# Optimization experiments

Hardware: AMD Instinct MI355X
Metric: run time of the kernel (lower is better)

## Reference

```python
import jax, jax.numpy as jnp
import numpy as np

IN_F = 1024   # in_features
OUT_F = 1024  # out_features
N = 32768     # flattened batch (prod of x.shape[:-1]))
K = 3         # clones per rewire -> denom = K + 1


def setup_inputs() -> dict:
    key = jax.random.key(0)
    k1, k2, k3, k4 = jax.random.split(key, 4)
    bound = 1.0 / np.sqrt(IN_F)
    x = jax.random.normal(k1, (N, IN_F), dtype=jnp.float32)
    # kaiming-uniform-ish init scale for weight, uniform(-bound,bound) for bias
    weight = jax.random.uniform(k2, (OUT_F, IN_F), dtype=jnp.float32,
                                minval=-bound, maxval=bound) * np.sqrt(3.0)
    bias = jax.random.uniform(k3, (OUT_F,), dtype=jnp.float32,
                              minval=-bound, maxval=bound)
    # one rewire per output row; clones are distinct from src (dead-neuron slots)
    rewire_rows = jnp.arange(OUT_F, dtype=jnp.int32)
    rewire_src = jax.random.randint(k4, (OUT_F,), 0, IN_F, dtype=jnp.int32)
    rewire_clones = (rewire_src[:, None] + jnp.arange(1, K + 1, dtype=jnp.int32)) % IN_F
    return {"x": x, "weight": weight, "bias": bias,
            "rewire_rows": rewire_rows, "rewire_src": rewire_src,
            "rewire_clones": rewire_clones}


def reference(x, weight, bias, rewire_rows, rewire_src, rewire_clones):
    # Plain linear part, shared by all output rows: y = x @ W^T + b
    base = x @ weight.T + bias                                  # [N, OUT_F]

    # Per-rewire correction. For rewire e on row r with src s and clones d_k
    # (denom = K+1), the torch loop replaces x[:, s] -> x[:, s]/denom and
    # x[:, d_k] -> x[:, s]/denom before the GEMV with weight[r].
    # Equivalent delta added to base[:, r] (indices within a rewire are disjoint):
    denom = rewire_clones.shape[1] + 1                          # K + 1
    xs = x[:, rewire_src]                                       # [N, R]
    new_val = xs / denom                                        # [N, R]
    w_src = weight[rewire_rows, rewire_src]                     # [R]
    delta = (new_val - xs) * w_src                              # src column change
    xc = x[:, rewire_clones]                                    # [N, R, K]
    wc = weight[rewire_rows[:, None], rewire_clones]            # [R, K]
    delta = delta + jnp.einsum('nrk,rk->nr', new_val[:, :, None] - xc, wc)

    # Scatter-add the deltas into their output rows (duplicates accumulate).
    return base.at[:, rewire_rows].add(delta)                   # [N, OUT_F]
```

## Files before the change

### kernel.cpp

```cpp
#include <hip/hip_runtime.h>

#define IN_F 1024
#define OUT_F 1024
#define NTOK 32768
#define BM 256
#define BN 256
#define BK 64
#define KT (IN_F / BK)

typedef __bf16 bf16;
typedef __bf16 bf16x4 __attribute__((ext_vector_type(4)));
typedef __bf16 bf16x8 __attribute__((ext_vector_type(8)));
typedef float f32x4 __attribute__((ext_vector_type(4)));

__global__ void build_wp(const float* __restrict__ W,
                         const int* __restrict__ rows,
                         const int* __restrict__ srcs,
                         const int* __restrict__ clones,
                         bf16* __restrict__ Wp) {
  const int r = blockIdx.x;
  const int row = rows[r];
  const int s = srcs[r];
  const int c0 = clones[3 * r + 0];
  const int c1 = clones[3 * r + 1];
  const int c2 = clones[3 * r + 2];
  const float* wr = W + (size_t)row * IN_F;
  const float fixv = 0.25f * (wr[s] + wr[c0] + wr[c1] + wr[c2]);

  const int col = threadIdx.x * 4;
  f32x4 v = *reinterpret_cast<const f32x4*>(wr + col);
  bf16x4 o;
#pragma unroll
  for (int j = 0; j < 4; ++j) {
    const int c = col + j;
    float f = v[j];
    if (c == c0 || c == c1 || c == c2) f = 0.0f;
    if (c == s) f = fixv;
    o[j] = (bf16)f;
  }
  *reinterpret_cast<bf16x4*>(Wp + (size_t)row * IN_F + col) = o;
}

__global__ __launch_bounds__(512, 2) void gemm_rewire(
    const float* __restrict__ X, const bf16* __restrict__ Wp,
    const float* __restrict__ bias, float* __restrict__ out) {
  extern __shared__ __align__(16) char smem[];

  const int tid = threadIdx.x;
  const int lane = tid & 63;
  const int w = tid >> 6;
  const int wrow = w >> 2;
  const int wcol = w & 3;

  const int bid = blockIdx.x;
  const int sq = bid >> 3;
  const int bm = (bid & 7) + 8 * (sq >> 2);
  const int bn = sq & 3;

  const float* gA = X + ((size_t)bm * BM + (tid >> 3)) * IN_F + (tid & 7) * 8;
  const int awbyte =
      ((tid >> 3) << 7) + ((((tid & 7) ^ ((tid >> 3) & 7))) << 4);

  const bf16* gB = Wp + ((size_t)bn * BN + w * 8 + (lane >> 3)) * IN_F +
                   (((lane & 7) ^ ((lane >> 3) & 7)) << 3);

  f32x4 acc[8][4];
#pragma unroll
  for (int n = 0; n < 4; ++n) {
    const float bv = bias[bn * BN + wcol * 64 + n * 16 + (lane & 15)];
#pragma unroll
    for (int m = 0; m < 8; ++m) acc[m][n] = (f32x4){bv, bv, bv, bv};
  }

  const int arow0 = wrow * 128 + (lane & 15);
  const int brow0 = wcol * 64 + (lane & 15);
  const int sl0 = lane >> 4;
  const int lx7 = lane & 7;

  f32x4 av[8];

  auto issueA = [&](int t) {
#pragma unroll
    for (int j = 0; j < 4; ++j) {
      const float* p = gA + (size_t)j * 64 * IN_F + (size_t)t * BK;
      av[2 * j] = *reinterpret_cast<const f32x4*>(p);
      av[2 * j + 1] = *reinterpret_cast<const f32x4*>(p + 4);
    }
  };
  auto writeA = [&](int buf) {
    char* base = smem + buf * 32768;
#pragma unroll
    for (int j = 0; j < 4; ++j) {
      bf16x8 o;
#pragma unroll
      for (int q = 0; q < 4; ++q) {
        o[q] = (bf16)av[2 * j][q];
        o[4 + q] = (bf16)av[2 * j + 1][q];
      }
      *reinterpret_cast<bf16x8*>(base + j * 8192 + awbyte) = o;
    }
  };
  auto issueB = [&](int t, int buf) {
    const bf16* g = gB + (size_t)t * BK;
    char* dst0 = smem + 65536 + buf * 32768 + w * 1024;
#pragma unroll
    for (int i = 0; i < 4; ++i) {
      __builtin_amdgcn_global_load_lds(
          (const __attribute__((address_space(1))) void*)(g +
                                                          (size_t)i * 64 * IN_F),
          (__attribute__((address_space(3))) void*)(dst0 + i * 8192), 16, 0, 0);
    }
  };
  auto compute = [&](int buf) {
    const char* A = smem + buf * 32768;
    const char* B = smem + 65536 + buf * 32768;
#pragma unroll
    for (int kk = 0; kk < 2; ++kk) {
      const int sl = sl0 + kk * 4;
      const int so = ((sl ^ lx7) << 4);
      bf16x8 af[8], bfr[4];
#pragma unroll
      for (int m = 0; m < 8; ++m)
        af[m] =
            *reinterpret_cast<const bf16x8*>(A + (arow0 + m * 16) * 128 + so);
#pragma unroll
      for (int n = 0; n < 4; ++n)
        bfr[n] =
            *reinterpret_cast<const bf16x8*>(B + (brow0 + n * 16) * 128 + so);
      __builtin_amdgcn_s_setprio(1);
#pragma unroll
      for (int m = 0; m < 8; ++m)
#pragma unroll
        for (int n = 0; n < 4; ++n)
          acc[m][n] = __builtin_amdgcn_mfma_f32_16x16x32_bf16(
              af[m], bfr[n], acc[m][n], 0, 0, 0);
      __builtin_amdgcn_s_setprio(0);
    }
  };

  issueA(0);
  issueB(0, 0);
  writeA(0);
  __syncthreads();

  for (int t = 0; t < KT; ++t) {
    const int db = t & 1;
    const bool more = (t + 1) < KT;
    if (more) {
      issueA(t + 1);
      issueB(t + 1, db ^ 1);
      __builtin_amdgcn_sched_barrier(0);
    }
    compute(db);
    if (more) {
      __builtin_amdgcn_sched_barrier(0);
      writeA(db ^ 1);
      __syncthreads();
    }
  }

  const int orow0 = bm * BM + wrow * 128 + (lane >> 4) * 4;
  const int ocol = bn * BN + wcol * 64 + (lane & 15);
#pragma unroll
  for (int m = 0; m < 8; ++m) {
#pragma unroll
    for (int n = 0; n < 4; ++n) {
      const f32x4 v = acc[m][n];
      const size_t base = (size_t)(orow0 + m * 16) * OUT_F + (ocol + n * 16);
#pragma unroll
      for (int i = 0; i < 4; ++i) out[base + (size_t)i * OUT_F] = v[i];
    }
  }
}

extern "C" void kernel_launch(void* const* d_in, const int* in_sizes, int n_in,
                              void* d_out, int out_size, void* d_ws,
                              size_t ws_size, hipStream_t stream) {
  const float* x = (const float*)d_in[0];
  const float* weight = (const float*)d_in[1];
  const float* bias = (const float*)d_in[2];
  const int* rrows = (const int*)d_in[3];
  const int* rsrc = (const int*)d_in[4];
  const int* rclones = (const int*)d_in[5];
  float* out = (float*)d_out;
  bf16* Wp = (bf16*)d_ws;

  (void)hipFuncSetAttribute((const void*)gemm_rewire,
                            hipFuncAttributeMaxDynamicSharedMemorySize, 131072);

  build_wp<<<dim3(OUT_F), dim3(256), 0, stream>>>(weight, rrows, rsrc, rclones,
                                                  Wp);
  gemm_rewire<<<dim3((NTOK / BM) * (OUT_F / BN)), dim3(512), 131072, stream>>>(
      x, Wp, bias, out);
}
```

Baseline: 106.3 us.

## Restructure GEMM main loop into fine-grained phased pipeline with manual waitcnts

Replaces the simple double-buffered K loop with a hand-scheduled loop unrolled by two K tiles. Each tile is split into four MFMA phases, and the A global loads, A LDS writes and B async LDS loads are interleaved in halves between those phases. Synchronisation uses explicit s_barrier and s_waitcnt vmcnt/lgkmcnt instead of __syncthreads. A is prefetched two tiles ahead in registers. The aim is to hide global latency and LDS traffic behind MFMA work, at the cost of more registers and fragile manual wait counts.

After: 105.6 us. Within noise of the previous version (-0.6%).

```diff
diff --git a/kernel.cpp b/kernel.cpp
--- a/kernel.cpp
+++ b/kernel.cpp
@@ -7,11 +7,17 @@
 #define BN 256
 #define BK 64
 #define KT (IN_F / BK)
+#define NITER (KT / 2)
 
 typedef __bf16 bf16;
 typedef __bf16 bf16x4 __attribute__((ext_vector_type(4)));
 typedef __bf16 bf16x8 __attribute__((ext_vector_type(8)));
 typedef float f32x4 __attribute__((ext_vector_type(4)));
+
+#define LDS_A0 0
+#define LDS_A1 32768
+#define LDS_B0 65536
+#define LDS_B1 98304
 
 __global__ void build_wp(const float* __restrict__ W,
                          const int* __restrict__ rows,
@@ -62,7 +68,7 @@
       ((tid >> 3) << 7) + ((((tid & 7) ^ ((tid >> 3) & 7))) << 4);
 
   const bf16* gB = Wp + ((size_t)bn * BN + w * 8 + (lane >> 3)) * IN_F +
-                   (((lane & 7) ^ ((lane >> 3) & 7)) << 3);
+                   (((lane & 7) ^ ((lane >> 3) & 7)) * 8);
 
   f32x4 acc[8][4];
 #pragma unroll
@@ -72,92 +78,140 @@
     for (int m = 0; m < 8; ++m) acc[m][n] = (f32x4){bv, bv, bv, bv};
   }
 
-  const int arow0 = wrow * 128 + (lane & 15);
-  const int brow0 = wcol * 64 + (lane & 15);
+  const int rl = lane & 15;
+  const int rx = rl & 7;
+  const int arow0 = wrow * 128 + rl;
+  const int brow0 = wcol * 64 + rl;
   const int sl0 = lane >> 4;
-  const int lx7 = lane & 7;
-
-  f32x4 av[8];
-
-  auto issueA = [&](int t) {
-#pragma unroll
-    for (int j = 0; j < 4; ++j) {
-      const float* p = gA + (size_t)j * 64 * IN_F + (size_t)t * BK;
-      av[2 * j] = *reinterpret_cast<const f32x4*>(p);
-      av[2 * j + 1] = *reinterpret_cast<const f32x4*>(p + 4);
-    }
-  };
-  auto writeA = [&](int buf) {
-    char* base = smem + buf * 32768;
-#pragma unroll
-    for (int j = 0; j < 4; ++j) {
+
+  bf16x8 bfr[4][2];
+  f32x4 aH0[4], aH1[4], aP0[4], aP1[4];
+
+  auto loadAhalf = [&](int t, int h, f32x4 (&v)[4]) {
+#pragma unroll
+    for (int jj = 0; jj < 2; ++jj) {
+      const float* p = gA + (size_t)(2 * h + jj) * 64 * IN_F + (size_t)t * BK;
+      v[2 * jj] = *reinterpret_cast<const f32x4*>(p);
+      v[2 * jj + 1] = *reinterpret_cast<const f32x4*>(p + 4);
+    }
+  };
+  auto writeAhalf = [&](int bufOff, int h, const f32x4 (&v)[4]) {
+#pragma unroll
+    for (int jj = 0; jj < 2; ++jj) {
       bf16x8 o;
 #pragma unroll
       for (int q = 0; q < 4; ++q) {
-        o[q] = (bf16)av[2 * j][q];
-        o[4 + q] = (bf16)av[2 * j + 1][q];
+        o[q] = (bf16)v[2 * jj][q];
+        o[4 + q] = (bf16)v[2 * jj + 1][q];
       }
-      *reinterpret_cast<bf16x8*>(base + j * 8192 + awbyte) = o;
-    }
-  };
-  auto issueB = [&](int t, int buf) {
-    const bf16* g = gB + (size_t)t * BK;
-    char* dst0 = smem + 65536 + buf * 32768 + w * 1024;
-#pragma unroll
-    for (int i = 0; i < 4; ++i) {
+      *reinterpret_cast<bf16x8*>(smem + bufOff + (2 * h + jj) * 8192 + awbyte) =
+          o;
+    }
+  };
+  auto issueBhalf = [&](int t, int bufOff, int h) {
+#pragma unroll
+    for (int ii = 0; ii < 2; ++ii) {
+      const int i = 2 * h + ii;
       __builtin_amdgcn_global_load_lds(
-          (const __attribute__((address_space(1))) void*)(g +
+          (const __attribute__((address_space(1))) void*)(gB + (size_t)t * BK +
                                                           (size_t)i * 64 * IN_F),
-          (__attribute__((address_space(3))) void*)(dst0 + i * 8192), 16, 0, 0);
-    }
-  };
-  auto compute = [&](int buf) {
-    const char* A = smem + buf * 32768;
-    const char* B = smem + 65536 + buf * 32768;
-#pragma unroll
-    for (int kk = 0; kk < 2; ++kk) {
-      const int sl = sl0 + kk * 4;
-      const int so = ((sl ^ lx7) << 4);
-      bf16x8 af[8], bfr[4];
-#pragma unroll
-      for (int m = 0; m < 8; ++m)
-        af[m] =
-            *reinterpret_cast<const bf16x8*>(A + (arow0 + m * 16) * 128 + so);
+          (__attribute__((address_space(3))) void*)(smem + bufOff + i * 8192 +
+                                                    w * 1024),
+          16, 0, 0);
+    }
+  };
+  auto readB = [&](int bufOff) {
+#pragma unroll
+    for (int n = 0; n < 4; ++n)
+#pragma unroll
+      for (int kk = 0; kk < 2; ++kk)
+        bfr[n][kk] = *reinterpret_cast<const bf16x8*>(
+            smem + bufOff + (brow0 + n * 16) * 128 +
+            (((kk * 4 + sl0) ^ rx) << 4));
+  };
+  auto phase = [&](int bufAOff, int m2, int ew) {
+    bf16x8 af[2][2];
+#pragma unroll
+    for (int dm = 0; dm < 2; ++dm)
+#pragma unroll
+      for (int kk = 0; kk < 2; ++kk)
+        af[dm][kk] = *reinterpret_cast<const bf16x8*>(
+            smem + bufAOff + (arow0 + (m2 + dm) * 16) * 128 +
+            (((kk * 4 + sl0) ^ rx) << 4));
+    __builtin_amdgcn_s_barrier();
+    asm volatile("s_waitcnt lgkmcnt(0)" ::: "memory");
+    __builtin_amdgcn_sched_barrier(0);
+    __builtin_amdgcn_s_setprio(1);
+#pragma unroll
+    for (int dm = 0; dm < 2; ++dm)
 #pragma unroll
       for (int n = 0; n < 4; ++n)
-        bfr[n] =
-            *reinterpret_cast<const bf16x8*>(B + (brow0 + n * 16) * 128 + so);
-      __builtin_amdgcn_s_setprio(1);
-#pragma unroll
-      for (int m = 0; m < 8; ++m)
-#pragma unroll
-        for (int n = 0; n < 4; ++n)
-          acc[m][n] = __builtin_amdgcn_mfma_f32_16x16x32_bf16(
-              af[m], bfr[n], acc[m][n], 0, 0, 0);
-      __builtin_amdgcn_s_setprio(0);
-    }
-  };
-
-  issueA(0);
-  issueB(0, 0);
-  writeA(0);
-  __syncthreads();
-
-  for (int t = 0; t < KT; ++t) {
-    const int db = t & 1;
-    const bool more = (t + 1) < KT;
-    if (more) {
-      issueA(t + 1);
-      issueB(t + 1, db ^ 1);
-      __builtin_amdgcn_sched_barrier(0);
-    }
-    compute(db);
-    if (more) {
-      __builtin_amdgcn_sched_barrier(0);
-      writeA(db ^ 1);
-      __syncthreads();
-    }
-  }
+#pragma unroll
+        for (int kk = 0; kk < 2; ++kk)
+          acc[m2 + dm][n] = __builtin_amdgcn_mfma_f32_16x16x32_bf16(
+              af[dm][kk], bfr[n][kk], acc[m2 + dm][n], 0, 0, 0);
+    __builtin_amdgcn_s_setprio(0);
+    if (ew == 8)
+      asm volatile("s_waitcnt vmcnt(8)" ::: "memory");
+    else if (ew == 1)
+      asm volatile("s_waitcnt vmcnt(0)" ::: "memory");
+    __builtin_amdgcn_s_barrier();
+  };
+
+  issueBhalf(0, LDS_B0, 0);
+  issueBhalf(0, LDS_B0, 1);
+  {
+    f32x4 aZ0[4], aZ1[4];
+    loadAhalf(0, 0, aZ0);
+    loadAhalf(0, 1, aZ1);
+    loadAhalf(1, 0, aP0);
+    loadAhalf(1, 1, aP1);
+    writeAhalf(LDS_A0, 0, aZ0);
+    writeAhalf(LDS_A0, 1, aZ1);
+  }
+  asm volatile("s_waitcnt vmcnt(8) lgkmcnt(0)" ::: "memory");
+  __builtin_amdgcn_s_barrier();
+
+#pragma unroll 1
+  for (int i = 0; i < NITER - 1; ++i) {
+    const int tb = 2 * i + 1, ta2 = 2 * i + 2, tb2 = 2 * i + 3;
+    writeAhalf(LDS_A1, 0, aP0);
+    issueBhalf(tb, LDS_B1, 0);
+    readB(LDS_B0);
+    phase(LDS_A0, 0, 0);
+    writeAhalf(LDS_A1, 1, aP1);
+    issueBhalf(tb, LDS_B1, 1);
+    loadAhalf(ta2, 0, aH0);
+    phase(LDS_A0, 2, 0);
+    loadAhalf(ta2, 1, aH1);
+    phase(LDS_A0, 4, 0);
+    phase(LDS_A0, 6, 8);
+    writeAhalf(LDS_A0, 0, aH0);
+    issueBhalf(ta2, LDS_B0, 0);
+    readB(LDS_B1);
+    phase(LDS_A1, 0, 0);
+    writeAhalf(LDS_A0, 1, aH1);
+    issueBhalf(ta2, LDS_B0, 1);
+    loadAhalf(tb2, 0, aP0);
+    phase(LDS_A1, 2, 0);
+    loadAhalf(tb2, 1, aP1);
+    phase(LDS_A1, 4, 0);
+    phase(LDS_A1, 6, 8);
+  }
+  writeAhalf(LDS_A1, 0, aP0);
+  issueBhalf(KT - 1, LDS_B1, 0);
+  readB(LDS_B0);
+  phase(LDS_A0, 0, 0);
+  writeAhalf(LDS_A1, 1, aP1);
+  issueBhalf(KT - 1, LDS_B1, 1);
+  phase(LDS_A0, 2, 0);
+  phase(LDS_A0, 4, 0);
+  phase(LDS_A0, 6, 1);
+  readB(LDS_B1);
+  phase(LDS_A1, 0, 0);
+  phase(LDS_A1, 2, 0);
+  phase(LDS_A1, 4, 0);
+  phase(LDS_A1, 6, 0);
 
   const int orow0 = bm * BM + wrow * 128 + (lane >> 4) * 4;
   const int ocol = bn * BN + wcol * 64 + (lane & 15);
```

## Pre-convert X to swizzled bf16 tiles and stream A via direct-to-LDS loads

Applied to the files above, without the earlier changes.

Adds a prep kernel that converts X from fp32 to bf16 once, in a pre-swizzled per-tile layout held in workspace. The GEMM can then load A tiles with global_load_lds like B, so it no longer converts in registers or writes A to LDS itself. Before, each X tile was read and converted four times, once per column block. The cost is an extra pass that writes and rereads a 64MB bf16 copy. It also depends on enough workspace, with a fallback to the old kernel when there isn't.

After: 116.6 us. +9.7%, slower.

```diff
diff --git a/kernel.cpp b/kernel.cpp
--- a/kernel.cpp
+++ b/kernel.cpp
@@ -41,8 +41,29 @@
   *reinterpret_cast<bf16x4*>(Wp + (size_t)row * IN_F + col) = o;
 }
 
-__global__ __launch_bounds__(512, 2) void gemm_rewire(
-    const float* __restrict__ X, const bf16* __restrict__ Wp,
+__global__ void prep_xb(const float* __restrict__ X, bf16* __restrict__ Xb) {
+  const int c = blockIdx.x * 256 + threadIdx.x;
+  const int q = c & 2047;
+  const int bmt = c >> 11;
+  const int bm = bmt >> 4;
+  const int t = bmt & 15;
+  const int row = q >> 3;
+  const int p = q & 7;
+  const int s = p ^ (row & 7);
+  const float* src = X + ((size_t)bm * BM + row) * IN_F + t * BK + s * 8;
+  const f32x4 a = *reinterpret_cast<const f32x4*>(src);
+  const f32x4 b = *reinterpret_cast<const f32x4*>(src + 4);
+  bf16x8 o;
+#pragma unroll
+  for (int j = 0; j < 4; ++j) {
+    o[j] = (bf16)a[j];
+    o[4 + j] = (bf16)b[j];
+  }
+  *reinterpret_cast<bf16x8*>(Xb + (size_t)c * 8) = o;
+}
+
+__global__ __launch_bounds__(512, 2) void gemm_bf(
+    const bf16* __restrict__ Xb, const bf16* __restrict__ Wp,
     const float* __restrict__ bias, float* __restrict__ out) {
   extern __shared__ __align__(16) char smem[];
 
@@ -57,12 +78,125 @@
   const int bm = (bid & 7) + 8 * (sq >> 2);
   const int bn = sq & 3;
 
+  const bf16* gA = Xb + (size_t)bm * (KT * 16384) + lane * 8;
+
+  const bf16* gB = Wp + ((size_t)bn * BN + w * 8 + (lane >> 3)) * IN_F +
+                   (((lane & 7) ^ ((lane >> 3) & 7)) * 8);
+
+  f32x4 acc[8][4];
+#pragma unroll
+  for (int n = 0; n < 4; ++n) {
+    const float bv = bias[bn * BN + wcol * 64 + n * 16 + (lane & 15)];
+#pragma unroll
+    for (int m = 0; m < 8; ++m) acc[m][n] = (f32x4){bv, bv, bv, bv};
+  }
+
+  const int rl = lane & 15;
+  const int rx = rl & 7;
+  const int arow0 = wrow * 128 + rl;
+  const int brow0 = wcol * 64 + rl;
+  const int sl0 = lane >> 4;
+
+  auto issueA = [&](int t, int buf) {
+    const bf16* g = gA + (size_t)t * 16384;
+#pragma unroll
+    for (int i = 0; i < 4; ++i) {
+      const int chunk = i * 8 + w;
+      __builtin_amdgcn_global_load_lds(
+          (const __attribute__((address_space(1))) void*)(g + chunk * 512),
+          (__attribute__((address_space(3))) void*)(smem + buf * 32768 +
+                                                    chunk * 1024),
+          16, 0, 0);
+    }
+  };
+  auto issueB = [&](int t, int buf) {
+    const bf16* g = gB + (size_t)t * BK;
+    char* dst0 = smem + 65536 + buf * 32768 + w * 1024;
+#pragma unroll
+    for (int i = 0; i < 4; ++i) {
+      __builtin_amdgcn_global_load_lds(
+          (const __attribute__((address_space(1))) void*)(g +
+                                                          (size_t)i * 64 * IN_F),
+          (__attribute__((address_space(3))) void*)(dst0 + i * 8192), 16, 0, 0);
+    }
+  };
+  auto compute = [&](int buf) {
+    const char* A = smem + buf * 32768;
+    const char* B = smem + 65536 + buf * 32768;
+#pragma unroll
+    for (int kk = 0; kk < 2; ++kk) {
+      const int so = (((kk * 4 + sl0) ^ rx) << 4);
+      bf16x8 af[8], bfr[4];
+#pragma unroll
+      for (int m = 0; m < 8; ++m)
+        af[m] =
+            *reinterpret_cast<const bf16x8*>(A + (arow0 + m * 16) * 128 + so);
+#pragma unroll
+      for (int n = 0; n < 4; ++n)
+        bfr[n] =
+            *reinterpret_cast<const bf16x8*>(B + (brow0 + n * 16) * 128 + so);
+      __builtin_amdgcn_s_setprio(1);
+#pragma unroll
+      for (int m = 0; m < 8; ++m)
+#pragma unroll
+        for (int n = 0; n < 4; ++n)
+          acc[m][n] = __builtin_amdgcn_mfma_f32_16x16x32_bf16(
+              af[m], bfr[n], acc[m][n], 0, 0, 0);
+      __builtin_amdgcn_s_setprio(0);
+    }
+  };
+
+  issueA(0, 0);
+  issueB(0, 0);
+  __syncthreads();
+
+  for (int t = 0; t < KT; ++t) {
+    const int db = t & 1;
+    if (t + 1 < KT) {
+      issueA(t + 1, db ^ 1);
+      issueB(t + 1, db ^ 1);
+      __builtin_amdgcn_sched_barrier(0);
+    }
+    compute(db);
+    __syncthreads();
+  }
+
+  const int orow0 = bm * BM + wrow * 128 + (lane >> 4) * 4;
+  const int ocol = bn * BN + wcol * 64 + (lane & 15);
+#pragma unroll
+  for (int m = 0; m < 8; ++m) {
+#pragma unroll
+    for (int n = 0; n < 4; ++n) {
+      const f32x4 v = acc[m][n];
+      const size_t base = (size_t)(orow0 + m * 16) * OUT_F + (ocol + n * 16);
+#pragma unroll
+      for (int i = 0; i < 4; ++i) out[base + (size_t)i * OUT_F] = v[i];
+    }
+  }
+}
+
+__global__ __launch_bounds__(512, 2) void gemm_r4(
+    const float* __restrict__ X, const bf16* __restrict__ Wp,
+    const float* __restrict__ bias, float* __restrict__ out) {
+  extern __shared__ __align__(16) char smem[];
+
+  const int tid = threadIdx.x;
+  const int lane = tid & 63;
+  const int w = tid >> 6;
+  const int wrow = w >> 2;
+  const int wcol = w & 3;
+
+  const int bid = blockIdx.x;
+  const int sq = bid >> 3;
+  const int bm = (bid & 7) + 8 * (sq >> 2);
+  const int bn = sq & 3;
+
   const float* gA = X + ((size_t)bm * BM + (tid >> 3)) * IN_F + (tid & 7) * 8;
   const int awbyte =
       ((tid >> 3) << 7) + ((((tid & 7) ^ ((tid >> 3) & 7))) << 4);
 
   const bf16* gB = Wp + ((size_t)bn * BN + w * 8 + (lane >> 3)) * IN_F +
-                   (((lane & 7) ^ ((lane >> 3) & 7)) << 3);
+                   (((lane & 7) ^ ((lane >> 3) & 7)) * 8);
 
   f32x4 acc[8][4];
 #pragma unroll
@@ -72,10 +206,11 @@
     for (int m = 0; m < 8; ++m) acc[m][n] = (f32x4){bv, bv, bv, bv};
   }
 
-  const int arow0 = wrow * 128 + (lane & 15);
-  const int brow0 = wcol * 64 + (lane & 15);
+  const int rl = lane & 15;
+  const int rx = rl & 7;
+  const int arow0 = wrow * 128 + rl;
+  const int brow0 = wcol * 64 + rl;
   const int sl0 = lane >> 4;
-  const int lx7 = lane & 7;
 
   f32x4 av[8];
 
@@ -116,8 +251,7 @@
     const char* B = smem + 65536 + buf * 32768;
 #pragma unroll
     for (int kk = 0; kk < 2; ++kk) {
-      const int sl = sl0 + kk * 4;
-      const int so = ((sl ^ lx7) << 4);
+      const int so = (((kk * 4 + sl0) ^ rx) << 4);
       bf16x8 af[8], bfr[4];
 #pragma unroll
       for (int m = 0; m < 8; ++m)
@@ -183,13 +317,25 @@
   const int* rsrc = (const int*)d_in[4];
   const int* rclones = (const int*)d_in[5];
   float* out = (float*)d_out;
+
   bf16* Wp = (bf16*)d_ws;
-
-  (void)hipFuncSetAttribute((const void*)gemm_rewire,
+  bf16* Xb = (bf16*)((char*)d_ws + (2u << 20));
+  const size_t need = (2u << 20) + (size_t)NTOK * IN_F * 2;
+
+  (void)hipFuncSetAttribute((const void*)gemm_bf,
+                            hipFuncAttributeMaxDynamicSharedMemorySize, 131072);
+  (void)hipFuncSetAttribute((const void*)gemm_r4,
                             hipFuncAttributeMaxDynamicSharedMemorySize, 131072);
 
   build_wp<<<dim3(OUT_F), dim3(256), 0, stream>>>(weight, rrows, rsrc, rclones,
                                                   Wp);
-  gemm_rewire<<<dim3((NTOK / BM) * (OUT_F / BN)), dim3(512), 131072, stream>>>(
-      x, Wp, bias, out);
-}
+  if (ws_size >= need) {
+    prep_xb<<<dim3((NTOK / BM) * KT * 2048 / 256), dim3(256), 0, stream>>>(x,
+                                                                           Xb);
+    gemm_bf<<<dim3((NTOK / BM) * (OUT_F / BN)), dim3(512), 131072, stream>>>(
+        Xb, Wp, bias, out);
+  } else {
+    gemm_r4<<<dim3((NTOK / BM) * (OUT_F / BN)), dim3(512), 131072, stream>>>(
+        x, Wp, bias, out);
+  }
+}
```
